# Performance work log

Hardware: AMD Instinct MI355X
Metric: run time of the kernel (lower is better)

Reference implementation:

```python
import jax, jax.numpy as jnp
import numpy as np

B, N, C, H = 16, 1024, 768, 12
HD = C // H
SCALE = HD ** -0.5


def setup_inputs() -> dict:
    key = jax.random.key(0)
    k1, k2, k3 = jax.random.split(key, 3)
    x = jax.random.normal(k1, (B, N, C), dtype=jnp.float32)
    W_qkv = jax.random.normal(k2, (C, 3 * C), dtype=jnp.float32) * (C ** -0.5)
    W_proj = jax.random.normal(k3, (C, C), dtype=jnp.float32) * (C ** -0.5)
    b_proj = jnp.zeros((C,), dtype=jnp.float32)
    return {"x": x, "W_qkv": W_qkv, "W_proj": W_proj, "b_proj": b_proj}


def reference(x, W_qkv, W_proj, b_proj):
    # qkv projection: [B, N, 3C] -> chunk into q, k, v
    qkv = x @ W_qkv
    q, k, v = jnp.split(qkv, 3, axis=-1)
    # reshape to [B, H, N, HD]
    q = q.reshape(B, N, H, HD).transpose(0, 2, 1, 3)
    k = k.reshape(B, N, H, HD).transpose(0, 2, 1, 3)
    v = v.reshape(B, N, H, HD).transpose(0, 2, 1, 3)
    # manual attention: scores, softmax, weighted sum
    attn = jnp.einsum("bhqd,bhkd->bhqk", q, k) * SCALE
    attn = jax.nn.softmax(attn, axis=-1)
    out = jnp.einsum("bhqk,bhkd->bhqd", attn, v)
    out = out.transpose(0, 2, 1, 3).reshape(B, N, C)
    # output projection
    return out @ W_proj + b_proj
```

## Files before the change

kernel.cpp:

```cpp
#include <hip/hip_runtime.h>

#define B_   16
#define NH   12
#define SEQ  1024
#define CD   768
#define HD_  64
#define MTOT (B_ * SEQ)
#define QSCALE 0.18033688f

typedef __attribute__((ext_vector_type(4)))  float  f32x4;
typedef __attribute__((ext_vector_type(16))) float  f32x16;
typedef __attribute__((ext_vector_type(8)))  __bf16 bf16x8;
typedef __attribute__((ext_vector_type(2)))  unsigned u32x2;

#define WAITV8 asm volatile("s_waitcnt vmcnt(8)" ::: "memory")
#define WAITV4 asm volatile("s_waitcnt vmcnt(4)" ::: "memory")
#define WAITV0 asm volatile("s_waitcnt vmcnt(0)" ::: "memory")
#define LGKM0  asm volatile("s_waitcnt lgkmcnt(0)" ::: "memory")
#define BAR    __builtin_amdgcn_s_barrier()
#define SB0    __builtin_amdgcn_sched_barrier(0)

__device__ __forceinline__ unsigned short f2bf(float f) {
  unsigned u = __float_as_uint(f);
  u = (u + 0x7FFFu + ((u >> 16) & 1u)) >> 16;
  return (unsigned short)u;
}

__device__ __forceinline__ void gload16(const void* g, void* l) {
  __builtin_amdgcn_global_load_lds(
      (const __attribute__((address_space(1))) void*)g,
      (__attribute__((address_space(3))) void*)l, 16, 0, 0);
}

__device__ __forceinline__ u32x2 pswap(unsigned x, unsigned y) {
  return __builtin_amdgcn_permlane32_swap(x, y, false, false);
}


__global__ void cvt_x_kernel(const float* __restrict__ in,
                             unsigned short* __restrict__ out, int n4) {
  int i = blockIdx.x * blockDim.x + threadIdx.x;
  if (i >= n4) return;
  float4 f = reinterpret_cast<const float4*>(in)[i];
  uint2 o;
  o.x = (unsigned)f2bf(f.x) | ((unsigned)f2bf(f.y) << 16);
  o.y = (unsigned)f2bf(f.z) | ((unsigned)f2bf(f.w) << 16);
  reinterpret_cast<uint2*>(out)[i] = o;
}

__global__ void transpose_cvt_kernel(const float* __restrict__ W,
                                     unsigned short* __restrict__ Wt,
                                     int K, int N) {
  __shared__ float tile[32][33];
  int j0 = blockIdx.x * 32, k0 = blockIdx.y * 32;
  int tx = threadIdx.x, ty = threadIdx.y;
  #pragma unroll
  for (int i = 0; i < 4; i++)
    tile[ty + 8 * i][tx] = W[(size_t)(k0 + ty + 8 * i) * N + j0 + tx];
  __syncthreads();
  #pragma unroll
  for (int i = 0; i < 4; i++)
    Wt[(size_t)(j0 + ty + 8 * i) * K + k0 + tx] = f2bf(tile[tx][ty + 8 * i]);
}


__device__ __forceinline__ bf16x8 ldsA64(const unsigned short* buf, int row, int g) {
  int byte = (row << 6) + ((g << 4) ^ (((row >> 1) & 3) << 4));
  return *reinterpret_cast<const bf16x8*>((const char*)buf + byte);
}
__device__ __forceinline__ bf16x8 lds128(const unsigned short* buf, int row, int cb) {
  int byte = (row << 7) + (cb ^ ((row & 7) << 4));
  return *reinterpret_cast<const bf16x8*>((const char*)buf + byte);
}


template <int MODE>
__global__ __launch_bounds__(256, 3)
void gemm128_kernel(const unsigned short* __restrict__ A,
                    const unsigned short* __restrict__ Bt,
                    unsigned short* __restrict__ qkvOut,
                    unsigned short* __restrict__ vtOut,
                    float* __restrict__ outF,
                    const float* __restrict__ bias) {
  constexpr int K = 768;
  __shared__ unsigned short sbuf[24576];
  unsigned short* const A0 = sbuf;
  unsigned short* const Bb0 = sbuf + 4096;
  unsigned short* const A1 = sbuf + 8192;
  unsigned short* const Bb1 = sbuf + 12288;
  unsigned short* const A2 = sbuf + 16384;
  unsigned short* const Bb2 = sbuf + 20480;

  const int tid = threadIdx.x;
  const int lane = tid & 63;
  const int wave = tid >> 6;
  const int wm = (wave >> 1) << 6;
  const int wn = (wave & 1) << 6;
  const int m0 = blockIdx.x << 7;
  const int j0 = blockIdx.y << 7;

  const int sr = tid >> 2;
  const int sc = (tid & 3) << 4;
  const int scs = sc ^ (((sr >> 1) & 3) << 4);

  f32x4 acc[4][4] = {};

  const char* const ab  = (const char*)(A  + (size_t)(m0 + sr) * K) + scs;
  const char* const ab2 = (const char*)(A  + (size_t)(m0 + sr + 64) * K) + scs;
  const char* const bb  = (const char*)(Bt + (size_t)(j0 + sr) * K) + scs;
  const char* const bb2 = (const char*)(Bt + (size_t)(j0 + sr + 64) * K) + scs;

  auto stageT = [&](int kt, unsigned short* Ad, unsigned short* Bd) {
    const int kb = kt * 64;
    gload16(ab  + kb, (char*)Ad + tid * 16);
    gload16(ab2 + kb, (char*)Ad + 4096 + tid * 16);
    gload16(bb  + kb, (char*)Bd + tid * 16);
    gload16(bb2 + kb, (char*)Bd + 4096 + tid * 16);
  };

  auto computeT = [&](const unsigned short* As, const unsigned short* Bs) {
    bf16x8 af[4], bf[4];
    const int g = lane >> 4;
    #pragma unroll
    for (int fr = 0; fr < 4; fr++) af[fr] = ldsA64(As, wm + fr * 16 + (lane & 15), g);
    #pragma unroll
    for (int fn = 0; fn < 4; fn++) bf[fn] = ldsA64(Bs, wn + fn * 16 + (lane & 15), g);
    #pragma unroll
    for (int fr = 0; fr < 4; fr++)
      #pragma unroll
      for (int fn = 0; fn < 4; fn++)
        acc[fr][fn] = __builtin_amdgcn_mfma_f32_16x16x32_bf16(af[fr], bf[fn],
                                                              acc[fr][fn], 0, 0, 0);
  };

  stageT(0, A0, Bb0);
  stageT(1, A1, Bb1);
  stageT(2, A2, Bb2);

  #pragma unroll 1
  for (int t = 0; t < 21; t += 3) {
    WAITV8; BAR; SB0;
    computeT(A0, Bb0);
    SB0; LGKM0; BAR;
    stageT(t + 3, A0, Bb0);

    WAITV8; BAR; SB0;
    computeT(A1, Bb1);
    SB0; LGKM0; BAR;
    stageT(t + 4, A1, Bb1);

    WAITV8; BAR; SB0;
    computeT(A2, Bb2);
    SB0; LGKM0; BAR;
    stageT(t + 5, A2, Bb2);
  }
  WAITV8; BAR; SB0;
  computeT(A0, Bb0);
  WAITV4; BAR; SB0;
  computeT(A1, Bb1);
  WAITV0; BAR; SB0;
  computeT(A2, Bb2);

  const int g4 = (lane >> 4) << 2;

  if (MODE == 0) {
    LGKM0; BAR;
    const bool secV = (j0 >= 1536);
    const float scale = (j0 < 768) ? QSCALE : 1.0f;
    char* const ct = (char*)sbuf;
    #pragma unroll
    for (int fr = 0; fr < 4; fr++) {
      #pragma unroll
      for (int fn = 0; fn < 4; fn++) {
        const int j_l = wn + fn * 16 + (lane & 15);
        #pragma unroll
        for (int r = 0; r < 4; r++) {
          const int m_l = wm + fr * 16 + g4 + r;
          const unsigned short v = f2bf(acc[fr][fn][r] * scale);
          const int addr = secV ? (j_l * 288 + m_l * 2) : (m_l * 288 + j_l * 2);
          *reinterpret_cast<unsigned short*>(ct + addr) = v;
        }
      }
    }
    LGKM0; BAR;
    const int c = tid & 15, r0 = tid >> 4;
    if (!secV) {
      char* const gb = (char*)qkvOut + (size_t)m0 * 4608 + j0 * 2 + c * 16;
      #pragma unroll
      for (int k = 0; k < 8; k++) {
        const int row = r0 + 16 * k;
        const uint4 d = *reinterpret_cast<const uint4*>(ct + row * 288 + c * 16);
        *reinterpret_cast<uint4*>(gb + (size_t)row * 4608) = d;
      }
    } else {
      const int b = m0 >> 10, nblk = (m0 & 1023) >> 7;
      const int h0 = (j0 - 1536) >> 6;
      char* const vb = (char*)vtOut +
          ((size_t)(b * NH + h0) * 65536 + (size_t)nblk * 8192) * 2 + c * 16;
      #pragma unroll
      for (int k = 0; k < 8; k++) {
        const int row = r0 + 16 * k;
        const uint4 d = *reinterpret_cast<const uint4*>(ct + row * 288 + c * 16);
        const size_t off = ((size_t)(row >> 6) * 65536 + (size_t)(row & 63) * 128) * 2;
        *reinterpret_cast<uint4*>(vb + off) = d;
      }
    }
  } else {
    #pragma unroll
    for (int fr = 0; fr < 4; fr++) {
      #pragma unroll
      for (int fn = 0; fn < 4; fn++) {
        const int jl = j0 + wn + fn * 16 + (lane & 15);
        const int mb = m0 + wm + fr * 16 + g4;
        const float bv = bias[jl];
        #pragma unroll
        for (int r = 0; r < 4; r++)
          outF[(size_t)(mb + r) * CD + jl] = acc[fr][fn][r] + bv;
      }
    }
  }
}


__global__ __launch_bounds__(256, 4)
void attn_kernel(const unsigned short* __restrict__ qkvB,
                 const unsigned short* __restrict__ Vt,
                 unsigned short* __restrict__ Og) {
  __shared__ unsigned short ldsbuf[16384];
  __shared__ float sStat[2][4][32];

  unsigned short* const K0 = ldsbuf;
  unsigned short* const V0 = ldsbuf + 4096;
  unsigned short* const K1 = ldsbuf + 8192;
  unsigned short* const V1 = ldsbuf + 12288;
  unsigned short* const Qs = ldsbuf + 8192;

  const int tid = threadIdx.x;
  const int lane = tid & 63;
  const int wave = tid >> 6;
  const int half = lane >> 5;
  const int q_l = lane & 31;
  const int bh = blockIdx.x;
  const int q0 = blockIdx.y * 128;
  const int b = bh / NH, head = bh - b * NH;

  const int sr = tid >> 3;
  const int scs = ((tid & 7) << 4) ^ ((sr & 7) << 4);

  const char* const xb_ = (const char*)qkvB + (size_t)b * 1024 * 4608;
  const int qoff = head * 128;
  const int koff = qoff + 1536;
  const char* const vb0 = (const char*)Vt + (size_t)bh * 131072;

  {
    #pragma unroll
    for (int i = 0; i < 4; i++)
      gload16(xb_ + (size_t)(q0 + sr + 32 * i) * 4608 + qoff + scs,
              (char*)Qs + (tid + 256 * i) * 16);
    gload16(xb_ + (size_t)sr * 4608 + koff + scs, (char*)K0 + tid * 16);
    gload16(xb_ + (size_t)(sr + 32) * 4608 + koff + scs, (char*)K0 + 4096 + tid * 16);
    gload16(vb0 + sr * 256 + scs, (char*)V0 + tid * 16);
    gload16(vb0 + (sr + 32) * 256 + scs, (char*)V0 + 4096 + tid * 16);
  }
  __syncthreads();

  bf16x8 qf[4];
  #pragma unroll
  for (int c = 0; c < 4; c++)
    qf[c] = lds128(Qs, wave * 32 + q_l, 32 * c + 16 * half);
  __syncthreads();

  f32x16 o0 = {}, o1 = {};
  float mrun = -1e30f, lrun = 0.f;

  for (int t = 0; t < 16; t++) {
    const unsigned short* const Kc = (t & 1) ? K1 : K0;
    const unsigned short* const Vc = (t & 1) ? V1 : V0;
    unsigned short* const Kn = (t & 1) ? K0 : K1;
    unsigned short* const Vn = (t & 1) ? V0 : V1;
    if (t < 15) {
      const int kv1 = (t + 1) * 64;
      const char* const vtile = vb0 + (kv1 >> 7) * 16384 + ((kv1 >> 6) & 1) * 128;
      gload16(xb_ + (size_t)(kv1 + sr) * 4608 + koff + scs, (char*)Kn + tid * 16);
      gload16(xb_ + (size_t)(kv1 + sr + 32) * 4608 + koff + scs,
              (char*)Kn + 4096 + tid * 16);
      gload16(vtile + sr * 256 + scs, (char*)Vn + tid * 16);
      gload16(vtile + (sr + 32) * 256 + scs, (char*)Vn + 4096 + tid * 16);
    }

    f32x16 s0 = {}, s1 = {};
    #pragma unroll
    for (int c = 0; c < 4; c++) {
      bf16x8 kf0 = lds128(Kc, q_l, 32 * c + 16 * half);
      bf16x8 kf1 = lds128(Kc, 32 + q_l, 32 * c + 16 * half);
      s0 = __builtin_amdgcn_mfma_f32_32x32x16_bf16(kf0, qf[c], s0, 0, 0, 0);
      s1 = __builtin_amdgcn_mfma_f32_32x32x16_bf16(kf1, qf[c], s1, 0, 0, 0);
    }

    float vmax = fmaxf(s0[0], s1[0]);
    #pragma unroll
    for (int r = 1; r < 16; r++) vmax = fmaxf(vmax, fmaxf(s0[r], s1[r]));
    {
      u32x2 mx = pswap(__float_as_uint(vmax), __float_as_uint(vmax));
      vmax = fmaxf(__uint_as_float(mx[0]), __uint_as_float(mx[1]));
    }

    if (!__all(vmax <= mrun + 8.0f)) {
      const float mnew = fmaxf(mrun, vmax);
      const float corr = __builtin_amdgcn_exp2f(mrun - mnew);
      mrun = mnew;
      lrun *= corr;
      if (lane < 32) sStat[0][wave][q_l] = corr;
      f32x4 c4[4];
      #pragma unroll
      for (int j = 0; j < 4; j++)
        c4[j] = *reinterpret_cast<const f32x4*>(&sStat[0][wave][4 * half + 8 * j]);
      #pragma unroll
      for (int r = 0; r < 16; r++) {
        const float cc = c4[r >> 2][r & 3];
        o0[r] *= cc;
        o1[r] *= cc;
      }
    }

    float tsum = 0.f;
    #pragma unroll
    for (int r = 0; r < 16; r++) {
      const float p0 = __builtin_amdgcn_exp2f(s0[r] - mrun);
      const float p1 = __builtin_amdgcn_exp2f(s1[r] - mrun);
      s0[r] = p0; s1[r] = p1;
      tsum += p0 + p1;
    }
    {
      u32x2 ts = pswap(__float_as_uint(tsum), __float_as_uint(tsum));
      tsum = __uint_as_float(ts[0]) + __uint_as_float(ts[1]);
    }
    lrun += tsum;

    unsigned pk[2][8];
    #pragma unroll
    for (int w = 0; w < 8; w++) {
      asm("v_cvt_pk_bf16_f32 %0, %1, %2"
          : "=v"(pk[0][w]) : "v"(s0[2 * w]), "v"(s0[2 * w + 1]));
      asm("v_cvt_pk_bf16_f32 %0, %1, %2"
          : "=v"(pk[1][w]) : "v"(s1[2 * w]), "v"(s1[2 * w + 1]));
    }

    #pragma unroll
    for (int c = 0; c < 4; c++) {
      const int st = c >> 1, cc = c & 1;
      u32x2 rA = pswap(pk[st][4 * cc + 0], pk[st][4 * cc + 2]);
      u32x2 rB = pswap(pk[st][4 * cc + 1], pk[st][4 * cc + 3]);
      union { unsigned u[4]; bf16x8 v; } pa;
      pa.u[0] = rA[0]; pa.u[1] = rB[0]; pa.u[2] = rA[1]; pa.u[3] = rB[1];
      bf16x8 vf0 = lds128(Vc, q_l, 32 * c + 16 * half);
      bf16x8 vf1 = lds128(Vc, 32 + q_l, 32 * c + 16 * half);
      o0 = __builtin_amdgcn_mfma_f32_32x32x16_bf16(pa.v, vf0, o0, 0, 0, 0);
      o1 = __builtin_amdgcn_mfma_f32_32x32x16_bf16(pa.v, vf1, o1, 0, 0, 0);
    }
    __syncthreads();
  }

  if (lane < 32) sStat[1][wave][q_l] = lrun;
  f32x4 rl4[4];
  #pragma unroll
  for (int j = 0; j < 4; j++) {
    f32x4 lv = *reinterpret_cast<const f32x4*>(&sStat[1][wave][4 * half + 8 * j]);
    #pragma unroll
    for (int e = 0; e < 4; e++) rl4[j][e] = __builtin_amdgcn_rcpf(lv[e]);
  }
  #pragma unroll
  for (int r = 0; r < 16; r++) {
    const int qq = q0 + wave * 32 + (r & 3) + 8 * (r >> 2) + 4 * half;
    const float rl = rl4[r >> 2][r & 3];
    const size_t base = ((size_t)b * SEQ + qq) * CD + head * HD_;
    Og[base + q_l]      = f2bf(o0[r] * rl);
    Og[base + 32 + q_l] = f2bf(o1[r] * rl);
  }
}


extern "C" void kernel_launch(void* const* d_in, const int* in_sizes, int n_in,
                              void* d_out, int out_size, void* d_ws, size_t ws_size,
                              hipStream_t stream) {
  const float* x     = (const float*)d_in[0];
  const float* Wqkv  = (const float*)d_in[1];
  const float* Wproj = (const float*)d_in[2];
  const float* bproj = (const float*)d_in[3];

  char* ws = (char*)d_ws;
  unsigned short* qkvB = (unsigned short*)(ws + 0);
  unsigned short* Vt   = (unsigned short*)(ws + 75497472);
  unsigned short* xb   = (unsigned short*)(ws + 100663296);
  unsigned short* ao   = (unsigned short*)(ws + 100663296);
  unsigned short* wqT  = (unsigned short*)(ws + 125829120);
  unsigned short* wpT  = (unsigned short*)(ws + 129368064);
  if (ws_size < 130547712ull) return;

  const int n4 = MTOT * CD / 4;
  cvt_x_kernel<<<n4 / 256, 256, 0, stream>>>(x, xb, n4);
  transpose_cvt_kernel<<<dim3(2304 / 32, 768 / 32), dim3(32, 8), 0, stream>>>(Wqkv, wqT, 768, 2304);
  transpose_cvt_kernel<<<dim3(768 / 32, 768 / 32), dim3(32, 8), 0, stream>>>(Wproj, wpT, 768, 768);

  gemm128_kernel<0><<<dim3(128, 18), 256, 0, stream>>>(xb, wqT, qkvB, Vt,
                                                       nullptr, nullptr);
  attn_kernel<<<dim3(B_ * NH, SEQ / 128), 256, 0, stream>>>(qkvB, Vt, ao);
  gemm128_kernel<1><<<dim3(128, 6), 256, 0, stream>>>(ao, wpT, nullptr, nullptr,
                                                      (float*)d_out, bproj);
}
```

Measured before the change: 197.6 us.

## Replace 128x128 GEMM tiles with 256x256 tiles using 512 threads and double buffering

Both projection GEMMs move from 128x128 tiles (256 threads, triple-buffered 64-wide K steps) to 256x256 tiles (512 threads, 8 waves, double-buffered 128-wide K steps), each wave holding 128x64 of output. The aim is more operand reuse per byte of LDS and global traffic, with the next stage's loads issued while MFMAs run and wave priority raised around the MFMA block. The epilogue now writes the QKV/V-transposed output in two 128-column passes through padded LDS. The cost is fewer blocks (576 and 192), which risks under-filling the 256 CUs, especially for the output projection, plus heavier register and LDS use.

```diff
diff --git a/kernel.cpp b/kernel.cpp
--- a/kernel.cpp
+++ b/kernel.cpp
@@ -14,7 +14,6 @@
 typedef __attribute__((ext_vector_type(2)))  unsigned u32x2;
 
 #define WAITV8 asm volatile("s_waitcnt vmcnt(8)" ::: "memory")
-#define WAITV4 asm volatile("s_waitcnt vmcnt(4)" ::: "memory")
 #define WAITV0 asm volatile("s_waitcnt vmcnt(0)" ::: "memory")
 #define LGKM0  asm volatile("s_waitcnt lgkmcnt(0)" ::: "memory")
 #define BAR    __builtin_amdgcn_s_barrier()
@@ -64,10 +63,6 @@
 }
 
 
-__device__ __forceinline__ bf16x8 ldsA64(const unsigned short* buf, int row, int g) {
-  int byte = (row << 6) + ((g << 4) ^ (((row >> 1) & 3) << 4));
-  return *reinterpret_cast<const bf16x8*>((const char*)buf + byte);
-}
 __device__ __forceinline__ bf16x8 lds128(const unsigned short* buf, int row, int cb) {
   int byte = (row << 7) + (cb ^ ((row & 7) << 4));
   return *reinterpret_cast<const bf16x8*>((const char*)buf + byte);
@@ -75,143 +70,170 @@
 
 
 template <int MODE>
-__global__ __launch_bounds__(256, 3)
-void gemm128_kernel(const unsigned short* __restrict__ A,
+__global__ __launch_bounds__(512, 2)
+void gemm256_kernel(const unsigned short* __restrict__ A,
                     const unsigned short* __restrict__ Bt,
                     unsigned short* __restrict__ qkvOut,
                     unsigned short* __restrict__ vtOut,
                     float* __restrict__ outF,
                     const float* __restrict__ bias) {
   constexpr int K = 768;
-  __shared__ unsigned short sbuf[24576];
-  unsigned short* const A0 = sbuf;
-  unsigned short* const Bb0 = sbuf + 4096;
-  unsigned short* const A1 = sbuf + 8192;
-  unsigned short* const Bb1 = sbuf + 12288;
-  unsigned short* const A2 = sbuf + 16384;
-  unsigned short* const Bb2 = sbuf + 20480;
+  __shared__ unsigned short lds[65536];
+  unsigned short* const A0 = lds;
+  unsigned short* const B0 = lds + 16384;
+  unsigned short* const A1 = lds + 32768;
+  unsigned short* const B1 = lds + 49152;
 
   const int tid = threadIdx.x;
   const int lane = tid & 63;
   const int wave = tid >> 6;
-  const int wm = (wave >> 1) << 6;
-  const int wn = (wave & 1) << 6;
-  const int m0 = blockIdx.x << 7;
-  const int j0 = blockIdx.y << 7;
-
-  const int sr = tid >> 2;
-  const int sc = (tid & 3) << 4;
-  const int scs = sc ^ (((sr >> 1) & 3) << 4);
-
-  f32x4 acc[4][4] = {};
-
-  const char* const ab  = (const char*)(A  + (size_t)(m0 + sr) * K) + scs;
-  const char* const ab2 = (const char*)(A  + (size_t)(m0 + sr + 64) * K) + scs;
-  const char* const bb  = (const char*)(Bt + (size_t)(j0 + sr) * K) + scs;
-  const char* const bb2 = (const char*)(Bt + (size_t)(j0 + sr + 64) * K) + scs;
+  const int wm = wave >> 2;
+  const int wn = wave & 3;
+  const int m0 = blockIdx.x << 8;
+  const int j0 = blockIdx.y << 8;
+
+  const int srow = tid >> 3;
+  const int scol = (tid & 7) << 4;
+  const int ssw = scol ^ ((srow & 7) << 4);
+
+  const char* const aS = (const char*)A  + (size_t)(m0 + srow) * (K * 2) + ssw;
+  const char* const bS = (const char*)Bt + (size_t)(j0 + srow) * (K * 2) + ssw;
+
+  f32x4 acc[8][4] = {};
 
   auto stageT = [&](int kt, unsigned short* Ad, unsigned short* Bd) {
-    const int kb = kt * 64;
-    gload16(ab  + kb, (char*)Ad + tid * 16);
-    gload16(ab2 + kb, (char*)Ad + 4096 + tid * 16);
-    gload16(bb  + kb, (char*)Bd + tid * 16);
-    gload16(bb2 + kb, (char*)Bd + 4096 + tid * 16);
+    const char* as = aS + kt * 128;
+    const char* bs = bS + kt * 128;
+    char* ad = (char*)Ad + tid * 16;
+    char* bd = (char*)Bd + tid * 16;
+    #pragma unroll
+    for (int p = 0; p < 4; p++) gload16(as + p * 98304, ad + p * 8192);
+    #pragma unroll
+    for (int p = 0; p < 4; p++) gload16(bs + p * 98304, bd + p * 8192);
   };
 
-  auto computeT = [&](const unsigned short* As, const unsigned short* Bs) {
-    bf16x8 af[4], bf[4];
-    const int g = lane >> 4;
-    #pragma unroll
-    for (int fr = 0; fr < 4; fr++) af[fr] = ldsA64(As, wm + fr * 16 + (lane & 15), g);
-    #pragma unroll
-    for (int fn = 0; fn < 4; fn++) bf[fn] = ldsA64(Bs, wn + fn * 16 + (lane & 15), g);
-    #pragma unroll
-    for (int fr = 0; fr < 4; fr++)
+  const int rl = lane & 15;
+  const int fcb = (lane >> 4) << 4;
+
+  auto iterT = [&](const unsigned short* Ax, const unsigned short* Bx,
+                   int kstage, unsigned short* Ad, unsigned short* Bd) {
+    bf16x8 bfr[2][4], af[2][8];
+    #pragma unroll
+    for (int kk = 0; kk < 2; kk++)
       #pragma unroll
       for (int fn = 0; fn < 4; fn++)
-        acc[fr][fn] = __builtin_amdgcn_mfma_f32_16x16x32_bf16(af[fr], bf[fn],
-                                                              acc[fr][fn], 0, 0, 0);
+        bfr[kk][fn] = lds128(Bx, wn * 64 + fn * 16 + rl, kk * 64 + fcb);
+    #pragma unroll
+    for (int kk = 0; kk < 2; kk++)
+      #pragma unroll
+      for (int fr = 0; fr < 8; fr++)
+        af[kk][fr] = lds128(Ax, wm * 128 + fr * 16 + rl, kk * 64 + fcb);
+    LGKM0; SB0;
+    BAR;
+    if (kstage >= 0) stageT(kstage, Ad, Bd);
+    SB0;
+    __builtin_amdgcn_s_setprio(1);
+    #pragma unroll
+    for (int kk = 0; kk < 2; kk++)
+      #pragma unroll
+      for (int fr = 0; fr < 8; fr++)
+        #pragma unroll
+        for (int fn = 0; fn < 4; fn++)
+          acc[fr][fn] = __builtin_amdgcn_mfma_f32_16x16x32_bf16(
+              af[kk][fr], bfr[kk][fn], acc[fr][fn], 0, 0, 0);
+    __builtin_amdgcn_s_setprio(0);
   };
 
-  stageT(0, A0, Bb0);
-  stageT(1, A1, Bb1);
-  stageT(2, A2, Bb2);
+  stageT(0, A0, B0);
+  stageT(1, A1, B1);
 
   #pragma unroll 1
-  for (int t = 0; t < 21; t += 3) {
+  for (int t = 0; t < 10; t += 2) {
     WAITV8; BAR; SB0;
-    computeT(A0, Bb0);
-    SB0; LGKM0; BAR;
-    stageT(t + 3, A0, Bb0);
-
+    iterT(A0, B0, t + 2, A0, B0);
     WAITV8; BAR; SB0;
-    computeT(A1, Bb1);
-    SB0; LGKM0; BAR;
-    stageT(t + 4, A1, Bb1);
-
-    WAITV8; BAR; SB0;
-    computeT(A2, Bb2);
-    SB0; LGKM0; BAR;
-    stageT(t + 5, A2, Bb2);
+    iterT(A1, B1, t + 3, A1, B1);
   }
   WAITV8; BAR; SB0;
-  computeT(A0, Bb0);
-  WAITV4; BAR; SB0;
-  computeT(A1, Bb1);
+  iterT(A0, B0, -1, nullptr, nullptr);
   WAITV0; BAR; SB0;
-  computeT(A2, Bb2);
+  iterT(A1, B1, -1, nullptr, nullptr);
 
   const int g4 = (lane >> 4) << 2;
 
   if (MODE == 0) {
-    LGKM0; BAR;
-    const bool secV = (j0 >= 1536);
-    const float scale = (j0 < 768) ? QSCALE : 1.0f;
-    char* const ct = (char*)sbuf;
-    #pragma unroll
-    for (int fr = 0; fr < 4; fr++) {
-      #pragma unroll
-      for (int fn = 0; fn < 4; fn++) {
-        const int j_l = wn + fn * 16 + (lane & 15);
-        #pragma unroll
-        for (int r = 0; r < 4; r++) {
-          const int m_l = wm + fr * 16 + g4 + r;
-          const unsigned short v = f2bf(acc[fr][fn][r] * scale);
-          const int addr = secV ? (j_l * 288 + m_l * 2) : (m_l * 288 + j_l * 2);
-          *reinterpret_cast<unsigned short*>(ct + addr) = v;
+    char* const ct = (char*)lds;
+    #pragma unroll
+    for (int p = 0; p < 2; p++) {
+      const int jw0 = j0 + p * 128;
+      const bool secV = (jw0 >= 1536);
+      const float scale = (jw0 < 768) ? QSCALE : 1.0f;
+      BAR;
+      if ((wn >> 1) == p) {
+        const int jb = (wn & 1) << 6;
+        if (!secV) {
+          #pragma unroll
+          for (int fr = 0; fr < 8; fr++)
+            #pragma unroll
+            for (int fn = 0; fn < 4; fn++) {
+              const int j_l = jb + fn * 16 + rl;
+              const int mb = wm * 128 + fr * 16 + g4;
+              #pragma unroll
+              for (int r = 0; r < 4; r++)
+                *reinterpret_cast<unsigned short*>(ct + (mb + r) * 304 + j_l * 2) =
+                    f2bf(acc[fr][fn][r] * scale);
+            }
+        } else {
+          #pragma unroll
+          for (int fr = 0; fr < 8; fr++)
+            #pragma unroll
+            for (int fn = 0; fn < 4; fn++) {
+              const int j_l = jb + fn * 16 + rl;
+              const int mb = wm * 128 + fr * 16 + g4;
+              uint2 pkd;
+              pkd.x = (unsigned)f2bf(acc[fr][fn][0]) |
+                      ((unsigned)f2bf(acc[fr][fn][1]) << 16);
+              pkd.y = (unsigned)f2bf(acc[fr][fn][2]) |
+                      ((unsigned)f2bf(acc[fr][fn][3]) << 16);
+              *reinterpret_cast<uint2*>(ct + j_l * 560 + mb * 2) = pkd;
+            }
         }
       }
-    }
-    LGKM0; BAR;
-    const int c = tid & 15, r0 = tid >> 4;
-    if (!secV) {
-      char* const gb = (char*)qkvOut + (size_t)m0 * 4608 + j0 * 2 + c * 16;
-      #pragma unroll
-      for (int k = 0; k < 8; k++) {
-        const int row = r0 + 16 * k;
-        const uint4 d = *reinterpret_cast<const uint4*>(ct + row * 288 + c * 16);
-        *reinterpret_cast<uint4*>(gb + (size_t)row * 4608) = d;
+      LGKM0; BAR;
+      if (!secV) {
+        const int c = tid & 15, r0 = tid >> 4;
+        char* const gb = (char*)qkvOut + (size_t)m0 * 4608 + jw0 * 2 + c * 16;
+        #pragma unroll
+        for (int k = 0; k < 8; k++) {
+          const int row = r0 + 32 * k;
+          const uint4 d = *reinterpret_cast<const uint4*>(ct + row * 304 + c * 16);
+          *reinterpret_cast<uint4*>(gb + (size_t)row * 4608) = d;
+        }
+      } else {
+        const int c = tid & 31, r0 = tid >> 5;
+        const int bidx = m0 >> 10;
+        const int nblk0 = (m0 & 1023) >> 7;
+        const int nb = nblk0 + (c >> 4);
+        const int mloc = (c * 8) & 127;
+        #pragma unroll
+        for (int k = 0; k < 8; k++) {
+          const int jr = r0 + 16 * k;
+          const int j_l = jw0 + jr;
+          const int h = (j_l - 1536) >> 6;
+          const int d = j_l & 63;
+          const size_t dst = ((size_t)((bidx * NH + h) * 8 + nb) * 64 + d) * 128 + mloc;
+          const uint4 v = *reinterpret_cast<const uint4*>(ct + jr * 560 + c * 16);
+          *reinterpret_cast<uint4*>((char*)vtOut + dst * 2) = v;
+        }
       }
-    } else {
-      const int b = m0 >> 10, nblk = (m0 & 1023) >> 7;
-      const int h0 = (j0 - 1536) >> 6;
-      char* const vb = (char*)vtOut +
-          ((size_t)(b * NH + h0) * 65536 + (size_t)nblk * 8192) * 2 + c * 16;
-      #pragma unroll
-      for (int k = 0; k < 8; k++) {
-        const int row = r0 + 16 * k;
-        const uint4 d = *reinterpret_cast<const uint4*>(ct + row * 288 + c * 16);
-        const size_t off = ((size_t)(row >> 6) * 65536 + (size_t)(row & 63) * 128) * 2;
-        *reinterpret_cast<uint4*>(vb + off) = d;
-      }
     }
   } else {
     #pragma unroll
-    for (int fr = 0; fr < 4; fr++) {
+    for (int fr = 0; fr < 8; fr++) {
       #pragma unroll
       for (int fn = 0; fn < 4; fn++) {
-        const int jl = j0 + wn + fn * 16 + (lane & 15);
-        const int mb = m0 + wm + fr * 16 + g4;
+        const int jl = j0 + wn * 64 + fn * 16 + rl;
+        const int mb = m0 + wm * 128 + fr * 16 + g4;
         const float bv = bias[jl];
         #pragma unroll
         for (int r = 0; r < 4; r++)
@@ -402,9 +424,9 @@
   transpose_cvt_kernel<<<dim3(2304 / 32, 768 / 32), dim3(32, 8), 0, stream>>>(Wqkv, wqT, 768, 2304);
   transpose_cvt_kernel<<<dim3(768 / 32, 768 / 32), dim3(32, 8), 0, stream>>>(Wproj, wpT, 768, 768);
 
-  gemm128_kernel<0><<<dim3(128, 18), 256, 0, stream>>>(xb, wqT, qkvB, Vt,
-                                                       nullptr, nullptr);
+  gemm256_kernel<0><<<dim3(64, 9), 512, 0, stream>>>(xb, wqT, qkvB, Vt,
+                                                     nullptr, nullptr);
   attn_kernel<<<dim3(B_ * NH, SEQ / 128), 256, 0, stream>>>(qkvB, Vt, ao);
-  gemm128_kernel<1><<<dim3(128, 6), 256, 0, stream>>>(ao, wpT, nullptr, nullptr,
-                                                      (float*)d_out, bproj);
-}
+  gemm256_kernel<1><<<dim3(64, 3), 512, 0, stream>>>(ao, wpT, nullptr, nullptr,
+                                                     (float*)d_out, bproj);
+}
```

New measurement: 244.2 us. 1.24x slower.

## Merge prep kernels and use 128x256 tiles for the QKV GEMM

Applied to the files above, without the earlier changes.

Folds the x conversion and both weight transposes into one prep kernel launch, removing two launches. Replaces the QKV projection with a dedicated kernel that uses 128x256 output tiles, where each wave computes 128x64 with 8x4 MFMA fragments, over a 3-stage global_load_lds pipeline. The larger tiles are meant to raise arithmetic intensity and cut redundant A-tile loads. In exchange the kernel needs more LDS and registers, which lowers occupancy to 2 blocks per CU, and the grid shrinks to 1152 blocks. The V-transpose epilogue is rewritten with packed stores.

```diff
diff --git a/kernel.cpp b/kernel.cpp
--- a/kernel.cpp
+++ b/kernel.cpp
@@ -13,12 +13,14 @@
 typedef __attribute__((ext_vector_type(8)))  __bf16 bf16x8;
 typedef __attribute__((ext_vector_type(2)))  unsigned u32x2;
 
-#define WAITV8 asm volatile("s_waitcnt vmcnt(8)" ::: "memory")
-#define WAITV4 asm volatile("s_waitcnt vmcnt(4)" ::: "memory")
-#define WAITV0 asm volatile("s_waitcnt vmcnt(0)" ::: "memory")
-#define LGKM0  asm volatile("s_waitcnt lgkmcnt(0)" ::: "memory")
-#define BAR    __builtin_amdgcn_s_barrier()
-#define SB0    __builtin_amdgcn_sched_barrier(0)
+#define WAITV12 asm volatile("s_waitcnt vmcnt(12)" ::: "memory")
+#define WAITV8  asm volatile("s_waitcnt vmcnt(8)" ::: "memory")
+#define WAITV6  asm volatile("s_waitcnt vmcnt(6)" ::: "memory")
+#define WAITV4  asm volatile("s_waitcnt vmcnt(4)" ::: "memory")
+#define WAITV0  asm volatile("s_waitcnt vmcnt(0)" ::: "memory")
+#define LGKM0   asm volatile("s_waitcnt lgkmcnt(0)" ::: "memory")
+#define BAR     __builtin_amdgcn_s_barrier()
+#define SB0     __builtin_amdgcn_sched_barrier(0)
 
 __device__ __forceinline__ unsigned short f2bf(float f) {
   unsigned u = __float_as_uint(f);
@@ -37,30 +39,40 @@
 }
 
 
-__global__ void cvt_x_kernel(const float* __restrict__ in,
-                             unsigned short* __restrict__ out, int n4) {
-  int i = blockIdx.x * blockDim.x + threadIdx.x;
-  if (i >= n4) return;
-  float4 f = reinterpret_cast<const float4*>(in)[i];
-  uint2 o;
-  o.x = (unsigned)f2bf(f.x) | ((unsigned)f2bf(f.y) << 16);
-  o.y = (unsigned)f2bf(f.z) | ((unsigned)f2bf(f.w) << 16);
-  reinterpret_cast<uint2*>(out)[i] = o;
-}
-
-__global__ void transpose_cvt_kernel(const float* __restrict__ W,
-                                     unsigned short* __restrict__ Wt,
-                                     int K, int N) {
+__global__ __launch_bounds__(256)
+void prep_kernel(const float* __restrict__ x,
+                 const float* __restrict__ Wqkv,
+                 const float* __restrict__ Wproj,
+                 unsigned short* __restrict__ xb,
+                 unsigned short* __restrict__ wqT,
+                 unsigned short* __restrict__ wpT) {
   __shared__ float tile[32][33];
-  int j0 = blockIdx.x * 32, k0 = blockIdx.y * 32;
-  int tx = threadIdx.x, ty = threadIdx.y;
-  #pragma unroll
-  for (int i = 0; i < 4; i++)
-    tile[ty + 8 * i][tx] = W[(size_t)(k0 + ty + 8 * i) * N + j0 + tx];
-  __syncthreads();
-  #pragma unroll
-  for (int i = 0; i < 4; i++)
-    Wt[(size_t)(j0 + ty + 8 * i) * K + k0 + tx] = f2bf(tile[tx][ty + 8 * i]);
+  const int bid = blockIdx.x;
+  const int tid = threadIdx.x;
+  if (bid < 12288) {
+    const int i = bid * 256 + tid;
+    float4 f = reinterpret_cast<const float4*>(x)[i];
+    uint2 o;
+    o.x = (unsigned)f2bf(f.x) | ((unsigned)f2bf(f.y) << 16);
+    o.y = (unsigned)f2bf(f.z) | ((unsigned)f2bf(f.w) << 16);
+    reinterpret_cast<uint2*>(xb)[i] = o;
+  } else {
+    const float* W;
+    unsigned short* Wt;
+    int N, b2;
+    if (bid < 12288 + 1728) { b2 = bid - 12288; W = Wqkv; Wt = wqT; N = 2304; }
+    else                    { b2 = bid - 14016; W = Wproj; Wt = wpT; N = 768; }
+    const int nb = N / 32;
+    const int j0 = (b2 % nb) * 32, k0 = (b2 / nb) * 32;
+    const int tx = tid & 31, ty = tid >> 5;
+    #pragma unroll
+    for (int i = 0; i < 4; i++)
+      tile[ty + 8 * i][tx] = W[(size_t)(k0 + ty + 8 * i) * N + j0 + tx];
+    __syncthreads();
+    #pragma unroll
+    for (int i = 0; i < 4; i++)
+      Wt[(size_t)(j0 + ty + 8 * i) * 768 + k0 + tx] = f2bf(tile[tx][ty + 8 * i]);
+  }
 }
 
 
@@ -71,6 +83,144 @@
 __device__ __forceinline__ bf16x8 lds128(const unsigned short* buf, int row, int cb) {
   int byte = (row << 7) + (cb ^ ((row & 7) << 4));
   return *reinterpret_cast<const bf16x8*>((const char*)buf + byte);
+}
+
+
+__global__ __launch_bounds__(256, 2)
+void gemm_qkv_kernel(const unsigned short* __restrict__ A,
+                     const unsigned short* __restrict__ Bt,
+                     unsigned short* __restrict__ qkvOut,
+                     unsigned short* __restrict__ vtOut) {
+  constexpr int K = 768;
+  __shared__ unsigned short sbuf[36864];
+
+  const int tid = threadIdx.x;
+  const int lane = tid & 63;
+  const int wave = tid >> 6;
+  const int m0 = blockIdx.x << 7;
+  const int j0 = blockIdx.y << 8;
+
+  const int sr = tid >> 2;
+  const int sc = (tid & 3) << 4;
+  const int scs = sc ^ (((sr >> 1) & 3) << 4);
+
+  f32x4 acc[8][4] = {};
+
+  const char* const aSrc = (const char*)(A  + (size_t)(m0 + sr) * K) + scs;
+  const char* const bSrc = (const char*)(Bt + (size_t)(j0 + sr) * K) + scs;
+
+  auto stageT = [&](int kt, int slot) {
+    const int kb = kt * 64;
+    char* ad = (char*)sbuf + slot * 8192 + tid * 16;
+    char* bd = (char*)sbuf + 24576 + slot * 16384 + tid * 16;
+    gload16(aSrc + kb, ad);
+    gload16(aSrc + kb + 98304, ad + 4096);
+    #pragma unroll
+    for (int p = 0; p < 4; p++)
+      gload16(bSrc + kb + p * 98304, bd + p * 4096);
+  };
+
+  const int g = lane >> 4;
+  const int rl = lane & 15;
+
+  auto computeT = [&](int slot) {
+    const unsigned short* As = sbuf + slot * 4096;
+    const unsigned short* Bs = sbuf + 12288 + slot * 8192;
+    bf16x8 bf[4], af[8];
+    #pragma unroll
+    for (int fn = 0; fn < 4; fn++) bf[fn] = ldsA64(Bs, wave * 64 + fn * 16 + rl, g);
+    #pragma unroll
+    for (int fr = 0; fr < 8; fr++) af[fr] = ldsA64(As, fr * 16 + rl, g);
+    #pragma unroll
+    for (int fr = 0; fr < 8; fr++)
+      #pragma unroll
+      for (int fn = 0; fn < 4; fn++)
+        acc[fr][fn] = __builtin_amdgcn_mfma_f32_16x16x32_bf16(af[fr], bf[fn],
+                                                              acc[fr][fn], 0, 0, 0);
+  };
+
+  stageT(0, 0);
+  stageT(1, 1);
+  stageT(2, 2);
+
+  #pragma unroll 1
+  for (int t = 0; t < 21; t += 3) {
+    WAITV12; BAR; SB0;
+    computeT(0);
+    SB0; LGKM0; BAR;
+    stageT(t + 3, 0);
+
+    WAITV12; BAR; SB0;
+    computeT(1);
+    SB0; LGKM0; BAR;
+    stageT(t + 4, 1);
+
+    WAITV12; BAR; SB0;
+    computeT(2);
+    SB0; LGKM0; BAR;
+    stageT(t + 5, 2);
+  }
+  WAITV12; BAR; SB0;
+  computeT(0);
+  WAITV6; BAR; SB0;
+  computeT(1);
+  WAITV0; BAR; SB0;
+  computeT(2);
+
+  const int g4 = g << 2;
+  BAR;
+  const bool secV = (j0 >= 1536);
+  const float scale = (j0 < 768) ? QSCALE : 1.0f;
+  char* const ct = (char*)sbuf;
+  if (!secV) {
+    #pragma unroll
+    for (int fr = 0; fr < 8; fr++)
+      #pragma unroll
+      for (int fn = 0; fn < 4; fn++) {
+        const int j_l = wave * 64 + fn * 16 + rl;
+        const int mb = fr * 16 + g4;
+        #pragma unroll
+        for (int r = 0; r < 4; r++)
+          *reinterpret_cast<unsigned short*>(ct + (mb + r) * 528 + j_l * 2) =
+              f2bf(acc[fr][fn][r] * scale);
+      }
+  } else {
+    #pragma unroll
+    for (int fr = 0; fr < 8; fr++)
+      #pragma unroll
+      for (int fn = 0; fn < 4; fn++) {
+        const int j_l = wave * 64 + fn * 16 + rl;
+        const int mb = fr * 16 + g4;
+        uint2 pkd;
+        pkd.x = (unsigned)f2bf(acc[fr][fn][0]) | ((unsigned)f2bf(acc[fr][fn][1]) << 16);
+        pkd.y = (unsigned)f2bf(acc[fr][fn][2]) | ((unsigned)f2bf(acc[fr][fn][3]) << 16);
+        *reinterpret_cast<uint2*>(ct + j_l * 264 + mb * 2) = pkd;
+      }
+  }
+  LGKM0; BAR;
+  if (!secV) {
+    const int c = tid & 31, r0 = tid >> 5;
+    char* const gb = (char*)qkvOut + (size_t)m0 * 4608 + j0 * 2 + c * 16;
+    #pragma unroll
+    for (int k = 0; k < 16; k++) {
+      const int row = r0 + 8 * k;
+      const uint4 d = *reinterpret_cast<const uint4*>(ct + row * 528 + c * 16);
+      *reinterpret_cast<uint4*>(gb + (size_t)row * 4608) = d;
+    }
+  } else {
+    const int c = tid & 15, r0 = tid >> 4;
+    const int bidx = m0 >> 10;
+    const int nblk = (m0 & 1023) >> 7;
+    #pragma unroll
+    for (int k = 0; k < 16; k++) {
+      const int jr = r0 + 16 * k;
+      const int h = ((j0 - 1536) >> 6) + (jr >> 6);
+      const int d = jr & 63;
+      const size_t dst = ((size_t)((bidx * NH + h) * 8 + nblk) * 64 + d) * 256 + c * 16;
+      const uint4 v = *reinterpret_cast<const uint4*>(ct + jr * 264 + c * 16);
+      *reinterpret_cast<uint4*>((char*)vtOut + dst) = v;
+    }
+  }
 }
 
 
@@ -78,8 +228,6 @@
 __global__ __launch_bounds__(256, 3)
 void gemm128_kernel(const unsigned short* __restrict__ A,
                     const unsigned short* __restrict__ Bt,
-                    unsigned short* __restrict__ qkvOut,
-                    unsigned short* __restrict__ vtOut,
                     float* __restrict__ outF,
                     const float* __restrict__ bias) {
   constexpr int K = 768;
@@ -162,61 +310,16 @@
   computeT(A2, Bb2);
 
   const int g4 = (lane >> 4) << 2;
-
-  if (MODE == 0) {
-    LGKM0; BAR;
-    const bool secV = (j0 >= 1536);
-    const float scale = (j0 < 768) ? QSCALE : 1.0f;
-    char* const ct = (char*)sbuf;
-    #pragma unroll
-    for (int fr = 0; fr < 4; fr++) {
-      #pragma unroll
-      for (int fn = 0; fn < 4; fn++) {
-        const int j_l = wn + fn * 16 + (lane & 15);
-        #pragma unroll
-        for (int r = 0; r < 4; r++) {
-          const int m_l = wm + fr * 16 + g4 + r;
-          const unsigned short v = f2bf(acc[fr][fn][r] * scale);
-          const int addr = secV ? (j_l * 288 + m_l * 2) : (m_l * 288 + j_l * 2);
-          *reinterpret_cast<unsigned short*>(ct + addr) = v;
-        }
-      }
-    }
-    LGKM0; BAR;
-    const int c = tid & 15, r0 = tid >> 4;
-    if (!secV) {
-      char* const gb = (char*)qkvOut + (size_t)m0 * 4608 + j0 * 2 + c * 16;
-      #pragma unroll
-      for (int k = 0; k < 8; k++) {
-        const int row = r0 + 16 * k;
-        const uint4 d = *reinterpret_cast<const uint4*>(ct + row * 288 + c * 16);
-        *reinterpret_cast<uint4*>(gb + (size_t)row * 4608) = d;
-      }
-    } else {
-      const int b = m0 >> 10, nblk = (m0 & 1023) >> 7;
-      const int h0 = (j0 - 1536) >> 6;
-      char* const vb = (char*)vtOut +
-          ((size_t)(b * NH + h0) * 65536 + (size_t)nblk * 8192) * 2 + c * 16;
-      #pragma unroll
-      for (int k = 0; k < 8; k++) {
-        const int row = r0 + 16 * k;
-        const uint4 d = *reinterpret_cast<const uint4*>(ct + row * 288 + c * 16);
-        const size_t off = ((size_t)(row >> 6) * 65536 + (size_t)(row & 63) * 128) * 2;
-        *reinterpret_cast<uint4*>(vb + off) = d;
-      }
-    }
-  } else {
-    #pragma unroll
-    for (int fr = 0; fr < 4; fr++) {
-      #pragma unroll
-      for (int fn = 0; fn < 4; fn++) {
-        const int jl = j0 + wn + fn * 16 + (lane & 15);
-        const int mb = m0 + wm + fr * 16 + g4;
-        const float bv = bias[jl];
-        #pragma unroll
-        for (int r = 0; r < 4; r++)
-          outF[(size_t)(mb + r) * CD + jl] = acc[fr][fn][r] + bv;
-      }
+  #pragma unroll
+  for (int fr = 0; fr < 4; fr++) {
+    #pragma unroll
+    for (int fn = 0; fn < 4; fn++) {
+      const int jl = j0 + wn + fn * 16 + (lane & 15);
+      const int mb = m0 + wm + fr * 16 + g4;
+      const float bv = bias[jl];
+      #pragma unroll
+      for (int r = 0; r < 4; r++)
+        outF[(size_t)(mb + r) * CD + jl] = acc[fr][fn][r] + bv;
     }
   }
 }
@@ -397,14 +500,8 @@
   unsigned short* wpT  = (unsigned short*)(ws + 129368064);
   if (ws_size < 130547712ull) return;
 
-  const int n4 = MTOT * CD / 4;
-  cvt_x_kernel<<<n4 / 256, 256, 0, stream>>>(x, xb, n4);
-  transpose_cvt_kernel<<<dim3(2304 / 32, 768 / 32), dim3(32, 8), 0, stream>>>(Wqkv, wqT, 768, 2304);
-  transpose_cvt_kernel<<<dim3(768 / 32, 768 / 32), dim3(32, 8), 0, stream>>>(Wproj, wpT, 768, 768);
-
-  gemm128_kernel<0><<<dim3(128, 18), 256, 0, stream>>>(xb, wqT, qkvB, Vt,
-                                                       nullptr, nullptr);
+  prep_kernel<<<14592, 256, 0, stream>>>(x, Wqkv, Wproj, xb, wqT, wpT);
+  gemm_qkv_kernel<<<dim3(128, 9), 256, 0, stream>>>(xb, wqT, qkvB, Vt);
   attn_kernel<<<dim3(B_ * NH, SEQ / 128), 256, 0, stream>>>(qkvB, Vt, ao);
-  gemm128_kernel<1><<<dim3(128, 6), 256, 0, stream>>>(ao, wpT, nullptr, nullptr,
-                                                      (float*)d_out, bproj);
-}
+  gemm128_kernel<1><<<dim3(128, 6), 256, 0, stream>>>(ao, wpT, (float*)d_out, bproj);
+}
```

New measurement: 189.5 us, median of 2. 4.1% less time.
